# Optimization experiments

Measured on AMD Instinct MI355X. Metric: run time of the kernel, lower is better.

## Reference

```python
import jax, jax.numpy as jnp
import numpy as np

B, T, E, H = 16, 2048, 1024, 128


def setup_inputs() -> dict:
    key = jax.random.key(0)
    kx, kk, kq, kv = jax.random.split(key, 4)
    x = jax.random.normal(kx, (B, T, E), dtype=jnp.float32)
    Wk = jax.random.normal(kk, (E, H), dtype=jnp.float32) / np.sqrt(E)
    Wq = jax.random.normal(kq, (E, H), dtype=jnp.float32) / np.sqrt(E)
    Wv = jax.random.normal(kv, (E, H), dtype=jnp.float32) / np.sqrt(E)
    mask = jnp.tril(jnp.ones((T, T), dtype=jnp.int32))  # causal mask; 0 => blocked
    return {"x": x, "mask": mask, "Wk": Wk, "Wq": Wq, "Wv": Wv}


def reference(x, mask, Wk, Wq, Wv):
    # k, q, v projections (Linear without bias)
    k = x @ Wk  # [B, T, H]
    q = x @ Wq
    v = x @ Wv
    scale = 1.0 / jnp.sqrt(jnp.asarray(H, dtype=x.dtype))
    wei = jnp.einsum("bth,bsh->bts", q, k) * scale  # [B, T, T]
    neg_inf = jnp.asarray(-jnp.inf, dtype=wei.dtype)
    wei = jnp.where(mask == 0, neg_inf, wei)
    wei = jax.nn.softmax(wei, axis=-1)
    out = jnp.einsum("bts,bsh->bth", wei, v)  # [B, T, H]
    return out
```

## Files before the change

kernel.cpp:

```cpp
#include <hip/hip_runtime.h>
#include <hip/hip_bf16.h>
#include <stdint.h>

typedef __attribute__((ext_vector_type(8))) short bf16x8;
typedef __attribute__((ext_vector_type(16))) float f32x16;
typedef __attribute__((ext_vector_type(4))) float f32x4;

__device__ __forceinline__ uint32_t cvt_pk_bf16(float a, float b){
  uint32_t r;
  asm volatile("v_cvt_pk_bf16_f32 %0, %1, %2" : "=v"(r) : "v"(a), "v"(b));
  return r;
}
__device__ __forceinline__ void permswap32(uint32_t &a, uint32_t &b){
  asm volatile("v_permlane32_swap_b32 %0, %1" : "+v"(a), "+v"(b));
}
__device__ __forceinline__ unsigned short f2bf(float f){
  uint32_t u = __float_as_uint(f);
  u += 0x7fff + ((u >> 16) & 1);
  return (unsigned short)(u >> 16);
}


__global__ void prep_w(const float* __restrict__ Wk, const float* __restrict__ Wq,
                       const float* __restrict__ Wv, unsigned short* __restrict__ Wt){
  int idx = blockIdx.x * 256 + threadIdx.x;
  int mat = idx >> 17;
  int r = idx & 131071;
  int h = r & 127;
  int e = r >> 7;
  const float* src = (mat == 0) ? Wq : (mat == 1) ? Wk : Wv;
  float v = src[r];
  if (mat == 0) v *= (1.4426950408889634f * 0.08838834764831845f);
  Wt[(mat * 128 + h) * 1024 + e] = f2bf(v);
}

#define LS 40
__global__ __launch_bounds__(256, 2) void proj_gemm(
    const float* __restrict__ x, const unsigned short* __restrict__ Wt,
    unsigned short* __restrict__ Qb, unsigned short* __restrict__ Kb,
    unsigned short* __restrict__ Vt){
  __shared__ __align__(16) unsigned short As[64 * LS];
  __shared__ __align__(16) unsigned short Bs[384 * LS];
  const int tid  = threadIdx.x;
  const int lane = tid & 63;
  const int w    = tid >> 6;
  const int lr   = lane & 15;
  const int lk   = lane >> 4;
  const int m0   = blockIdx.x * 64;

  f32x4 acc[4][6];
  #pragma unroll
  for (int i = 0; i < 4; ++i)
    #pragma unroll
    for (int jj = 0; jj < 6; ++jj) acc[i][jj] = (f32x4){0.f, 0.f, 0.f, 0.f};

  float4 areg[2];
  bf16x8 breg[6];
  #pragma unroll
  for (int i = 0; i < 2; ++i){
    int idx = i * 256 + tid; int row = idx >> 3, kp = idx & 7;
    areg[i] = *(const float4*)(x + (size_t)(m0 + row) * 1024 + kp * 4);
  }
  #pragma unroll
  for (int i = 0; i < 6; ++i){
    int idx = i * 256 + tid; int row = idx >> 2, pp = idx & 3;
    breg[i] = *(const bf16x8*)(Wt + (size_t)row * 1024 + pp * 8);
  }

  for (int ks = 0; ks < 32; ++ks){
    __syncthreads();
    #pragma unroll
    for (int i = 0; i < 2; ++i){
      int idx = i * 256 + tid; int row = idx >> 3, kp = idx & 7;
      uint32_t lo = cvt_pk_bf16(areg[i].x, areg[i].y);
      uint32_t hi = cvt_pk_bf16(areg[i].z, areg[i].w);
      *(uint2*)((char*)As + row * (LS * 2) + kp * 8) = make_uint2(lo, hi);
    }
    #pragma unroll
    for (int i = 0; i < 6; ++i){
      int idx = i * 256 + tid; int row = idx >> 2, pp = idx & 3;
      *(bf16x8*)((char*)Bs + row * (LS * 2) + pp * 16) = breg[i];
    }
    __syncthreads();
    if (ks + 1 < 32){
      int ko = (ks + 1) * 32;
      #pragma unroll
      for (int i = 0; i < 2; ++i){
        int idx = i * 256 + tid; int row = idx >> 3, kp = idx & 7;
        areg[i] = *(const float4*)(x + (size_t)(m0 + row) * 1024 + ko + kp * 4);
      }
      #pragma unroll
      for (int i = 0; i < 6; ++i){
        int idx = i * 256 + tid; int row = idx >> 2, pp = idx & 3;
        breg[i] = *(const bf16x8*)(Wt + (size_t)row * 1024 + ko + pp * 8);
      }
    }
    bf16x8 af[4], bfr[6];
    #pragma unroll
    for (int am = 0; am < 4; ++am)
      af[am] = *(const bf16x8*)((char*)As + (am * 16 + lr) * (LS * 2) + lk * 16);
    #pragma unroll
    for (int bn = 0; bn < 6; ++bn)
      bfr[bn] = *(const bf16x8*)((char*)Bs + (w * 96 + bn * 16 + lr) * (LS * 2) + lk * 16);
    #pragma unroll
    for (int am = 0; am < 4; ++am)
      #pragma unroll
      for (int bn = 0; bn < 6; ++bn)
        acc[am][bn] = __builtin_amdgcn_mfma_f32_16x16x32_bf16(af[am], bfr[bn], acc[am][bn], 0, 0, 0);
  }

  const int b  = m0 >> 11;
  const int t0 = m0 & 2047;
  #pragma unroll
  for (int am = 0; am < 4; ++am){
    #pragma unroll
    for (int bn = 0; bn < 6; ++bn){
      int c0   = w * 96 + bn * 16;
      int mat  = c0 >> 7;
      int hcol = (c0 & 127) + lr;
      int tr   = t0 + am * 16 + lk * 4;
      f32x4 v = acc[am][bn];
      if (mat <= 1){
        unsigned short* dst = (mat == 0) ? Qb : Kb;
        size_t base = (size_t)(b * 64 + (tr >> 5)) * 4096 + (size_t)(hcol >> 4) * 512 + (hcol & 15);
        #pragma unroll
        for (int jj = 0; jj < 4; ++jj)
          dst[base + (size_t)((tr + jj) & 31) * 16] = f2bf(v[jj]);
      } else {
        ushort4 pk;
        pk.x = f2bf(v[0]); pk.y = f2bf(v[1]); pk.z = f2bf(v[2]); pk.w = f2bf(v[3]);
        size_t addr = (size_t)((b * 64 + (tr >> 5)) * 4 + (hcol >> 5)) * 1024
                    + (size_t)((tr >> 4) & 1) * 512 + (size_t)(hcol & 31) * 16 + (tr & 15);
        *(ushort4*)(Vt + addr) = pk;
      }
    }
  }
}

__global__ __launch_bounds__(256, 2) void attn(
    const unsigned short* __restrict__ Qf, const unsigned short* __restrict__ Kf,
    const unsigned short* __restrict__ Vf, float* __restrict__ out){
  __shared__ float comb[32][132];
  __shared__ float msh[4][32];
  __shared__ float lsh[4][32];

  const int tid  = threadIdx.x;
  const int lane = tid & 63;
  const int w    = tid >> 6;
  const int bid  = blockIdx.x;
  const int xcd  = bid & 7;
  const int k    = bid >> 3;
  const int a    = k & 31;
  const int mdx  = k >> 5;
  const int b    = xcd * 2 + (mdx >> 1);
  const int c    = (mdx & 1) ? a : 63 - a;
  const int r0   = c * 32;
  const int q5   = lane & 31;
  const int hi   = lane >> 5;

  bf16x8 qf[8];
  const unsigned short* qp = Qf + (size_t)(b * 64 + c) * 4096 + q5 * 16 + hi * 8;
  #pragma unroll
  for (int f = 0; f < 8; ++f) qf[f] = *(const bf16x8*)(qp + f * 512);

  f32x16 oacc[4];
  #pragma unroll
  for (int i = 0; i < 4; ++i) oacc[i] = (f32x16)(0.f);
  float m = -1e30f, l = 0.f;

  const unsigned short* kb = Kf + (size_t)b * 64 * 4096;
  const unsigned short* vb = Vf + (size_t)b * 64 * 4096;

  bf16x8 kf[8];
  if (w <= c){
    const unsigned short* kp = kb + (size_t)w * 4096 + q5 * 16 + hi * 8;
    #pragma unroll
    for (int f = 0; f < 8; ++f) kf[f] = *(const bf16x8*)(kp + f * 512);
  }

  for (int t = w; t <= c; t += 4){
    f32x16 sacc = (f32x16)(0.f);
    #pragma unroll
    for (int f = 0; f < 8; ++f)
      sacc = __builtin_amdgcn_mfma_f32_32x32x16_bf16(kf[f], qf[f], sacc, 0, 0, 0);
    if (t + 4 <= c){
      const unsigned short* kp = kb + (size_t)(t + 4) * 4096 + q5 * 16 + hi * 8;
      #pragma unroll
      for (int f = 0; f < 8; ++f) kf[f] = *(const bf16x8*)(kp + f * 512);
    }
    bf16x8 vf[8];
    const unsigned short* vp = vb + (size_t)t * 4096 + q5 * 16 + hi * 8;
    #pragma unroll
    for (int ht = 0; ht < 4; ++ht)
      #pragma unroll
      for (int sf = 0; sf < 2; ++sf)
        vf[ht * 2 + sf] = *(const bf16x8*)(vp + ht * 1024 + sf * 512);

    float sv[16];
    #pragma unroll
    for (int r = 0; r < 16; ++r) sv[r] = sacc[r];
    if (t == c){
      #pragma unroll
      for (int r = 0; r < 16; ++r){
        int srow = (r & 3) + 8 * (r >> 2) + 4 * hi;
        if (srow > q5) sv[r] = -1e30f;
      }
    }
    float pm = sv[0];
    #pragma unroll
    for (int r = 1; r < 16; ++r) pm = fmaxf(pm, sv[r]);
    pm = fmaxf(pm, __shfl_xor(pm, 32));
    if (!__all(pm - m <= 8.0f)){
      float mn = fmaxf(m, pm);
      float al = exp2f(m - mn);
      #pragma unroll
      for (int i = 0; i < 4; ++i) oacc[i] *= al;
      l *= al;
      m = mn;
    }
    float pv[16]; float ts = 0.f;
    #pragma unroll
    for (int r = 0; r < 16; ++r){ pv[r] = exp2f(sv[r] - m); ts += pv[r]; }
    ts += __shfl_xor(ts, 32);
    l += ts;
    uint32_t w0 = cvt_pk_bf16(pv[0],  pv[1]);
    uint32_t w2 = cvt_pk_bf16(pv[4],  pv[5]);  permswap32(w0, w2);
    uint32_t w1 = cvt_pk_bf16(pv[2],  pv[3]);
    uint32_t w3 = cvt_pk_bf16(pv[6],  pv[7]);  permswap32(w1, w3);
    uint32_t w4 = cvt_pk_bf16(pv[8],  pv[9]);
    uint32_t w6 = cvt_pk_bf16(pv[12], pv[13]); permswap32(w4, w6);
    uint32_t w5 = cvt_pk_bf16(pv[10], pv[11]);
    uint32_t w7 = cvt_pk_bf16(pv[14], pv[15]); permswap32(w5, w7);
    union { uint32_t u[4]; bf16x8 v; } pf0u, pf1u;
    pf0u.u[0] = w0; pf0u.u[1] = w1; pf0u.u[2] = w2; pf0u.u[3] = w3;
    pf1u.u[0] = w4; pf1u.u[1] = w5; pf1u.u[2] = w6; pf1u.u[3] = w7;
    #pragma unroll
    for (int ht = 0; ht < 4; ++ht){
      oacc[ht] = __builtin_amdgcn_mfma_f32_32x32x16_bf16(vf[ht * 2 + 0], pf0u.v, oacc[ht], 0, 0, 0);
      oacc[ht] = __builtin_amdgcn_mfma_f32_32x32x16_bf16(vf[ht * 2 + 1], pf1u.v, oacc[ht], 0, 0, 0);
    }
  }

  if (hi == 0){ msh[w][q5] = m; lsh[w][q5] = l; }
  __syncthreads();
  {
    float mv0 = msh[0][q5], mv1 = msh[1][q5], mv2 = msh[2][q5], mv3 = msh[3][q5];
    float lv0 = lsh[0][q5], lv1 = lsh[1][q5], lv2 = lsh[2][q5], lv3 = lsh[3][q5];
    float mfm = fmaxf(fmaxf(mv0, mv1), fmaxf(mv2, mv3));
    float lf  = lv0 * exp2f(mv0 - mfm) + lv1 * exp2f(mv1 - mfm)
              + lv2 * exp2f(mv2 - mfm) + lv3 * exp2f(mv3 - mfm);
    float s = exp2f(m - mfm) / lf;
    #pragma unroll
    for (int ht = 0; ht < 4; ++ht) oacc[ht] *= s;
  }
  #pragma unroll 1
  for (int rr = 0; rr < 4; ++rr){
    if (w == rr){
      #pragma unroll
      for (int ht = 0; ht < 4; ++ht)
        #pragma unroll
        for (int r4 = 0; r4 < 4; ++r4){
          int hh = ht * 32 + 8 * r4 + 4 * hi;
          float4 add;
          add.x = oacc[ht][r4 * 4 + 0]; add.y = oacc[ht][r4 * 4 + 1];
          add.z = oacc[ht][r4 * 4 + 2]; add.w = oacc[ht][r4 * 4 + 3];
          float* p = &comb[q5][hh];
          if (rr == 0) *(float4*)p = add;
          else { float4 cur = *(const float4*)p;
                 cur.x += add.x; cur.y += add.y; cur.z += add.z; cur.w += add.w;
                 *(float4*)p = cur; }
        }
    }
    __syncthreads();
  }
  float* obase = out + ((size_t)b * 2048 + r0) * 128;
  #pragma unroll
  for (int it = 0; it < 4; ++it){
    int row = it * 8 + (tid >> 5);
    int col = (tid & 31) * 4;
    *(float4*)(obase + row * 128 + col) = *(const float4*)&comb[row][col];
  }
}

extern "C" void kernel_launch(void* const* d_in, const int* in_sizes, int n_in,
                              void* d_out, int out_size, void* d_ws, size_t ws_size,
                              hipStream_t stream){
  const float* x  = (const float*)d_in[0];
  const float* Wk = (const float*)d_in[2];
  const float* Wq = (const float*)d_in[3];
  const float* Wv = (const float*)d_in[4];
  char* ws = (char*)d_ws;
  unsigned short* Wt = (unsigned short*)(ws);
  unsigned short* Qb = (unsigned short*)(ws + (1ull  << 20));
  unsigned short* Kb = (unsigned short*)(ws + (9ull  << 20));
  unsigned short* Vt = (unsigned short*)(ws + (17ull << 20));
  float* out = (float*)d_out;

  hipLaunchKernelGGL(prep_w,    dim3(1536), dim3(256), 0, stream, Wk, Wq, Wv, Wt);
  hipLaunchKernelGGL(proj_gemm, dim3(512),  dim3(256), 0, stream, x, Wt, Qb, Kb, Vt);
  hipLaunchKernelGGL(attn,      dim3(1024), dim3(256), 0, stream, Qb, Kb, Vt, out);
}
```

Baseline: 89.07 us.

## Pre-swizzle weights into MFMA fragment layout and drop LDS staging in projection GEMM

The weight prep kernel now writes W in a fragment-tiled order, so each lane can load its bf16x8 MFMA operand straight from global memory. The projection GEMM drops shared memory and both barriers per k-step. Each wave loads its own x rows and weight fragments directly into registers, double-buffered in registers. The M tile is halved to 32 rows, the grid doubles to 1024 blocks, and launch bounds rise to 3 blocks per CU. This removes LDS traffic and synchronisation, at the cost of x being reloaded redundantly by all four waves and more global and L2 traffic for the weights.

```diff
diff --git a/kernel.cpp b/kernel.cpp
--- a/kernel.cpp
+++ b/kernel.cpp
@@ -24,95 +24,110 @@
 __global__ void prep_w(const float* __restrict__ Wk, const float* __restrict__ Wq,
                        const float* __restrict__ Wv, unsigned short* __restrict__ Wt){
   int idx = blockIdx.x * 256 + threadIdx.x;
-  int mat = idx >> 17;
-  int r = idx & 131071;
-  int h = r & 127;
-  int e = r >> 7;
+  int fid = idx >> 9;
+  int within = idx & 511;
+  int nlo = within >> 5;
+  int elo = within & 31;
+  int kq = fid / 24;
+  int nq = fid - kq * 24;
+  int n  = nq * 16 + nlo;
+  int e  = kq * 32 + elo;
+  int mat = n >> 7;
+  int h   = n & 127;
   const float* src = (mat == 0) ? Wq : (mat == 1) ? Wk : Wv;
-  float v = src[r];
+  float v = src[e * 128 + h];
   if (mat == 0) v *= (1.4426950408889634f * 0.08838834764831845f);
-  Wt[(mat * 128 + h) * 1024 + e] = f2bf(v);
-}
-
-#define LS 40
-__global__ __launch_bounds__(256, 2) void proj_gemm(
+  Wt[idx] = f2bf(v);
+}
+
+__global__ __launch_bounds__(256, 3) void proj_gemm(
     const float* __restrict__ x, const unsigned short* __restrict__ Wt,
     unsigned short* __restrict__ Qb, unsigned short* __restrict__ Kb,
     unsigned short* __restrict__ Vt){
-  __shared__ __align__(16) unsigned short As[64 * LS];
-  __shared__ __align__(16) unsigned short Bs[384 * LS];
   const int tid  = threadIdx.x;
   const int lane = tid & 63;
   const int w    = tid >> 6;
   const int lr   = lane & 15;
   const int lk   = lane >> 4;
-  const int m0   = blockIdx.x * 64;
-
-  f32x4 acc[4][6];
-  #pragma unroll
-  for (int i = 0; i < 4; ++i)
+  const int m0   = blockIdx.x * 32;
+
+  f32x4 acc[2][6];
+  #pragma unroll
+  for (int i = 0; i < 2; ++i)
     #pragma unroll
     for (int jj = 0; jj < 6; ++jj) acc[i][jj] = (f32x4){0.f, 0.f, 0.f, 0.f};
 
-  float4 areg[2];
-  bf16x8 breg[6];
-  #pragma unroll
-  for (int i = 0; i < 2; ++i){
-    int idx = i * 256 + tid; int row = idx >> 3, kp = idx & 7;
-    areg[i] = *(const float4*)(x + (size_t)(m0 + row) * 1024 + kp * 4);
-  }
-  #pragma unroll
-  for (int i = 0; i < 6; ++i){
-    int idx = i * 256 + tid; int row = idx >> 2, pp = idx & 3;
-    breg[i] = *(const bf16x8*)(Wt + (size_t)row * 1024 + pp * 8);
+  const float* xp = x + (size_t)(m0 + lr) * 1024 + lk * 8;
+  const unsigned short* bp = Wt + lr * 32 + lk * 8;
+
+  union BU { uint32_t u[4]; bf16x8 v; };
+
+  bf16x8 af0, af1, bcur0, bcur1, bcur2, bcur3, bcur4, bcur5;
+  {
+    float4 a00 = *(const float4*)(xp);
+    float4 a01 = *(const float4*)(xp + 4);
+    float4 a10 = *(const float4*)(xp + 16 * 1024);
+    float4 a11 = *(const float4*)(xp + 16 * 1024 + 4);
+    const unsigned short* bk = bp + (size_t)(w * 6) * 512;
+    bcur0 = *(const bf16x8*)(bk + 0 * 512);
+    bcur1 = *(const bf16x8*)(bk + 1 * 512);
+    bcur2 = *(const bf16x8*)(bk + 2 * 512);
+    bcur3 = *(const bf16x8*)(bk + 3 * 512);
+    bcur4 = *(const bf16x8*)(bk + 4 * 512);
+    bcur5 = *(const bf16x8*)(bk + 5 * 512);
+    BU u0; u0.u[0] = cvt_pk_bf16(a00.x, a00.y); u0.u[1] = cvt_pk_bf16(a00.z, a00.w);
+           u0.u[2] = cvt_pk_bf16(a01.x, a01.y); u0.u[3] = cvt_pk_bf16(a01.z, a01.w);
+    af0 = u0.v;
+    BU u1; u1.u[0] = cvt_pk_bf16(a10.x, a10.y); u1.u[1] = cvt_pk_bf16(a10.z, a10.w);
+           u1.u[2] = cvt_pk_bf16(a11.x, a11.y); u1.u[3] = cvt_pk_bf16(a11.z, a11.w);
+    af1 = u1.v;
   }
 
   for (int ks = 0; ks < 32; ++ks){
-    __syncthreads();
-    #pragma unroll
-    for (int i = 0; i < 2; ++i){
-      int idx = i * 256 + tid; int row = idx >> 3, kp = idx & 7;
-      uint32_t lo = cvt_pk_bf16(areg[i].x, areg[i].y);
-      uint32_t hi = cvt_pk_bf16(areg[i].z, areg[i].w);
-      *(uint2*)((char*)As + row * (LS * 2) + kp * 8) = make_uint2(lo, hi);
-    }
-    #pragma unroll
-    for (int i = 0; i < 6; ++i){
-      int idx = i * 256 + tid; int row = idx >> 2, pp = idx & 3;
-      *(bf16x8*)((char*)Bs + row * (LS * 2) + pp * 16) = breg[i];
-    }
-    __syncthreads();
-    if (ks + 1 < 32){
-      int ko = (ks + 1) * 32;
-      #pragma unroll
-      for (int i = 0; i < 2; ++i){
-        int idx = i * 256 + tid; int row = idx >> 3, kp = idx & 7;
-        areg[i] = *(const float4*)(x + (size_t)(m0 + row) * 1024 + ko + kp * 4);
-      }
-      #pragma unroll
-      for (int i = 0; i < 6; ++i){
-        int idx = i * 256 + tid; int row = idx >> 2, pp = idx & 3;
-        breg[i] = *(const bf16x8*)(Wt + (size_t)row * 1024 + ko + pp * 8);
-      }
-    }
-    bf16x8 af[4], bfr[6];
-    #pragma unroll
-    for (int am = 0; am < 4; ++am)
-      af[am] = *(const bf16x8*)((char*)As + (am * 16 + lr) * (LS * 2) + lk * 16);
-    #pragma unroll
-    for (int bn = 0; bn < 6; ++bn)
-      bfr[bn] = *(const bf16x8*)((char*)Bs + (w * 96 + bn * 16 + lr) * (LS * 2) + lk * 16);
-    #pragma unroll
-    for (int am = 0; am < 4; ++am)
-      #pragma unroll
-      for (int bn = 0; bn < 6; ++bn)
-        acc[am][bn] = __builtin_amdgcn_mfma_f32_16x16x32_bf16(af[am], bfr[bn], acc[am][bn], 0, 0, 0);
+    float4 a00, a01, a10, a11;
+    bf16x8 bn0, bn1, bn2, bn3, bn4, bn5;
+    const bool more = (ks + 1) < 32;
+    if (more){
+      const float* xk = xp + (ks + 1) * 32;
+      a00 = *(const float4*)(xk);
+      a01 = *(const float4*)(xk + 4);
+      a10 = *(const float4*)(xk + 16 * 1024);
+      a11 = *(const float4*)(xk + 16 * 1024 + 4);
+      const unsigned short* bk = bp + (size_t)((ks + 1) * 24 + w * 6) * 512;
+      bn0 = *(const bf16x8*)(bk + 0 * 512);
+      bn1 = *(const bf16x8*)(bk + 1 * 512);
+      bn2 = *(const bf16x8*)(bk + 2 * 512);
+      bn3 = *(const bf16x8*)(bk + 3 * 512);
+      bn4 = *(const bf16x8*)(bk + 4 * 512);
+      bn5 = *(const bf16x8*)(bk + 5 * 512);
+    }
+    acc[0][0] = __builtin_amdgcn_mfma_f32_16x16x32_bf16(af0, bcur0, acc[0][0], 0, 0, 0);
+    acc[1][0] = __builtin_amdgcn_mfma_f32_16x16x32_bf16(af1, bcur0, acc[1][0], 0, 0, 0);
+    acc[0][1] = __builtin_amdgcn_mfma_f32_16x16x32_bf16(af0, bcur1, acc[0][1], 0, 0, 0);
+    acc[1][1] = __builtin_amdgcn_mfma_f32_16x16x32_bf16(af1, bcur1, acc[1][1], 0, 0, 0);
+    acc[0][2] = __builtin_amdgcn_mfma_f32_16x16x32_bf16(af0, bcur2, acc[0][2], 0, 0, 0);
+    acc[1][2] = __builtin_amdgcn_mfma_f32_16x16x32_bf16(af1, bcur2, acc[1][2], 0, 0, 0);
+    acc[0][3] = __builtin_amdgcn_mfma_f32_16x16x32_bf16(af0, bcur3, acc[0][3], 0, 0, 0);
+    acc[1][3] = __builtin_amdgcn_mfma_f32_16x16x32_bf16(af1, bcur3, acc[1][3], 0, 0, 0);
+    acc[0][4] = __builtin_amdgcn_mfma_f32_16x16x32_bf16(af0, bcur4, acc[0][4], 0, 0, 0);
+    acc[1][4] = __builtin_amdgcn_mfma_f32_16x16x32_bf16(af1, bcur4, acc[1][4], 0, 0, 0);
+    acc[0][5] = __builtin_amdgcn_mfma_f32_16x16x32_bf16(af0, bcur5, acc[0][5], 0, 0, 0);
+    acc[1][5] = __builtin_amdgcn_mfma_f32_16x16x32_bf16(af1, bcur5, acc[1][5], 0, 0, 0);
+    if (more){
+      BU u0; u0.u[0] = cvt_pk_bf16(a00.x, a00.y); u0.u[1] = cvt_pk_bf16(a00.z, a00.w);
+             u0.u[2] = cvt_pk_bf16(a01.x, a01.y); u0.u[3] = cvt_pk_bf16(a01.z, a01.w);
+      af0 = u0.v;
+      BU u1; u1.u[0] = cvt_pk_bf16(a10.x, a10.y); u1.u[1] = cvt_pk_bf16(a10.z, a10.w);
+             u1.u[2] = cvt_pk_bf16(a11.x, a11.y); u1.u[3] = cvt_pk_bf16(a11.z, a11.w);
+      af1 = u1.v;
+      bcur0 = bn0; bcur1 = bn1; bcur2 = bn2; bcur3 = bn3; bcur4 = bn4; bcur5 = bn5;
+    }
   }
 
   const int b  = m0 >> 11;
   const int t0 = m0 & 2047;
   #pragma unroll
-  for (int am = 0; am < 4; ++am){
+  for (int am = 0; am < 2; ++am){
     #pragma unroll
     for (int bn = 0; bn < 6; ++bn){
       int c0   = w * 96 + bn * 16;
@@ -297,6 +312,6 @@
   float* out = (float*)d_out;
 
   hipLaunchKernelGGL(prep_w,    dim3(1536), dim3(256), 0, stream, Wk, Wq, Wv, Wt);
-  hipLaunchKernelGGL(proj_gemm, dim3(512),  dim3(256), 0, stream, x, Wt, Qb, Kb, Vt);
+  hipLaunchKernelGGL(proj_gemm, dim3(1024), dim3(256), 0, stream, x, Wt, Qb, Kb, Vt);
   hipLaunchKernelGGL(attn,      dim3(1024), dim3(256), 0, stream, Qb, Kb, Vt, out);
 }
```

Result: slower. 148.9 us (+67.1%).

## Stream projection GEMM tiles via direct global-to-LDS loads with multi-buffering

Applied to the files above, without the earlier changes.

The projection GEMM now copies x and the weight tiles straight into LDS with global_load_lds, replacing the register-staged loads and LDS stores. x uses a triple buffer and Wt a double buffer, so only one barrier per k-step is needed and loads overlap MFMA work. prep_w now writes the weights pre-swizzled into MFMA fragment order, and the fp32 x is converted to bf16 after the LDS read. The change also raises wave priority around the MFMA block. In exchange LDS use grows, which may limit occupancy, and the hand-written vmcnt waits must exactly match the number of loads in flight.

```diff
diff --git a/kernel.cpp b/kernel.cpp
--- a/kernel.cpp
+++ b/kernel.cpp
@@ -19,33 +19,41 @@
   u += 0x7fff + ((u >> 16) & 1);
   return (unsigned short)(u >> 16);
 }
+__device__ __forceinline__ void gload16(const void* g, void* l){
+  __builtin_amdgcn_global_load_lds((const __attribute__((address_space(1))) void*)g,
+                                   (__attribute__((address_space(3))) void*)l, 16, 0, 0);
+}
 
 
 __global__ void prep_w(const float* __restrict__ Wk, const float* __restrict__ Wq,
                        const float* __restrict__ Wv, unsigned short* __restrict__ Wt){
   int idx = blockIdx.x * 256 + threadIdx.x;
-  int mat = idx >> 17;
-  int r = idx & 131071;
-  int h = r & 127;
-  int e = r >> 7;
+  int frag = idx >> 9;
+  int r    = idx & 511;
+  int ln   = r >> 3;
+  int j    = r & 7;
+  int kq = frag / 24;
+  int nq = frag - kq * 24;
+  int n  = nq * 16 + (ln & 15);
+  int e  = kq * 32 + (ln >> 4) * 8 + j;
+  int mat = n >> 7;
+  int h   = n & 127;
   const float* src = (mat == 0) ? Wq : (mat == 1) ? Wk : Wv;
-  float v = src[r];
+  float v = src[e * 128 + h];
   if (mat == 0) v *= (1.4426950408889634f * 0.08838834764831845f);
-  Wt[(mat * 128 + h) * 1024 + e] = f2bf(v);
-}
-
-#define LS 40
+  Wt[idx] = f2bf(v);
+}
+
 __global__ __launch_bounds__(256, 2) void proj_gemm(
     const float* __restrict__ x, const unsigned short* __restrict__ Wt,
     unsigned short* __restrict__ Qb, unsigned short* __restrict__ Kb,
     unsigned short* __restrict__ Vt){
-  __shared__ __align__(16) unsigned short As[64 * LS];
-  __shared__ __align__(16) unsigned short Bs[384 * LS];
+  __shared__ __align__(16) float          As[3][2048];
+  __shared__ __align__(16) unsigned short Bs[2][12288];
+
   const int tid  = threadIdx.x;
   const int lane = tid & 63;
   const int w    = tid >> 6;
-  const int lr   = lane & 15;
-  const int lk   = lane >> 4;
   const int m0   = blockIdx.x * 64;
 
   f32x4 acc[4][6];
@@ -54,63 +62,70 @@
     #pragma unroll
     for (int jj = 0; jj < 6; ++jj) acc[i][jj] = (f32x4){0.f, 0.f, 0.f, 0.f};
 
-  float4 areg[2];
-  bf16x8 breg[6];
-  #pragma unroll
-  for (int i = 0; i < 2; ++i){
-    int idx = i * 256 + tid; int row = idx >> 3, kp = idx & 7;
-    areg[i] = *(const float4*)(x + (size_t)(m0 + row) * 1024 + kp * 4);
-  }
-  #pragma unroll
-  for (int i = 0; i < 6; ++i){
-    int idx = i * 256 + tid; int row = idx >> 2, pp = idx & 3;
-    breg[i] = *(const bf16x8*)(Wt + (size_t)row * 1024 + pp * 8);
-  }
+  const int lt0 = (lane >> 1), lt1 = 32 + (lane >> 1);
+  const int arow0 = w * 16 + (lt0 & 15), akk0 = (lt0 >> 4) * 8 + (lane & 1) * 4;
+  const int arow1 = w * 16 + (lt1 & 15), akk1 = (lt1 >> 4) * 8 + (lane & 1) * 4;
+  const float* asrc0 = x + (size_t)(m0 + arow0) * 1024 + akk0;
+  const float* asrc1 = x + (size_t)(m0 + arow1) * 1024 + akk1;
+  const unsigned short* bsrc = Wt + (size_t)lane * 8;
+
+  #define STAGE_A(kt, buf) {                                              \
+    gload16(asrc0 + (kt) * 32, &As[buf][(2 * w + 0) * 256]);              \
+    gload16(asrc1 + (kt) * 32, &As[buf][(2 * w + 1) * 256]);              \
+  }
+  #define STAGE_B(kt, buf) {                                              \
+    _Pragma("unroll")                                                     \
+    for (int jf = 0; jf < 6; ++jf){                                       \
+      int f = w * 6 + jf;                                                 \
+      gload16(bsrc + ((size_t)(kt) * 24 + f) * 512, &Bs[buf][f * 512]);   \
+    }                                                                     \
+  }
+
+  union BU { uint32_t u[4]; bf16x8 v; };
+
+  STAGE_B(0, 0);
+  STAGE_A(0, 0);
+  STAGE_A(1, 1);
+  asm volatile("s_waitcnt vmcnt(2)" ::: "memory");
+  __builtin_amdgcn_s_barrier();
+  __builtin_amdgcn_sched_barrier(0);
 
   for (int ks = 0; ks < 32; ++ks){
-    __syncthreads();
-    #pragma unroll
-    for (int i = 0; i < 2; ++i){
-      int idx = i * 256 + tid; int row = idx >> 3, kp = idx & 7;
-      uint32_t lo = cvt_pk_bf16(areg[i].x, areg[i].y);
-      uint32_t hi = cvt_pk_bf16(areg[i].z, areg[i].w);
-      *(uint2*)((char*)As + row * (LS * 2) + kp * 8) = make_uint2(lo, hi);
-    }
-    #pragma unroll
-    for (int i = 0; i < 6; ++i){
-      int idx = i * 256 + tid; int row = idx >> 2, pp = idx & 3;
-      *(bf16x8*)((char*)Bs + row * (LS * 2) + pp * 16) = breg[i];
-    }
-    __syncthreads();
-    if (ks + 1 < 32){
-      int ko = (ks + 1) * 32;
-      #pragma unroll
-      for (int i = 0; i < 2; ++i){
-        int idx = i * 256 + tid; int row = idx >> 3, kp = idx & 7;
-        areg[i] = *(const float4*)(x + (size_t)(m0 + row) * 1024 + ko + kp * 4);
-      }
-      #pragma unroll
-      for (int i = 0; i < 6; ++i){
-        int idx = i * 256 + tid; int row = idx >> 2, pp = idx & 3;
-        breg[i] = *(const bf16x8*)(Wt + (size_t)row * 1024 + ko + pp * 8);
-      }
-    }
-    bf16x8 af[4], bfr[6];
+    const int bcur = ks & 1, bnxt = bcur ^ 1;
+    const int acur = ks % 3, anxt2 = (ks + 2) % 3;
+    const int kb = (ks + 1 < 32) ? ks + 1 : 31;
+    const int ka = (ks + 2 < 32) ? ks + 2 : 31;
+    STAGE_B(kb, bnxt);
+    STAGE_A(ka, anxt2);
+    bf16x8 af[4];
+    #pragma unroll
+    for (int am = 0; am < 4; ++am){
+      float4 lo = *(const float4*)&As[acur][am * 512 + lane * 8];
+      float4 hi = *(const float4*)&As[acur][am * 512 + lane * 8 + 4];
+      BU u; u.u[0] = cvt_pk_bf16(lo.x, lo.y); u.u[1] = cvt_pk_bf16(lo.z, lo.w);
+            u.u[2] = cvt_pk_bf16(hi.x, hi.y); u.u[3] = cvt_pk_bf16(hi.z, hi.w);
+      af[am] = u.v;
+    }
+    bf16x8 bf[6];
+    #pragma unroll
+    for (int bn = 0; bn < 6; ++bn)
+      bf[bn] = *(const bf16x8*)&Bs[bcur][(w * 6 + bn) * 512 + lane * 8];
+    __builtin_amdgcn_s_setprio(1);
     #pragma unroll
     for (int am = 0; am < 4; ++am)
-      af[am] = *(const bf16x8*)((char*)As + (am * 16 + lr) * (LS * 2) + lk * 16);
-    #pragma unroll
-    for (int bn = 0; bn < 6; ++bn)
-      bfr[bn] = *(const bf16x8*)((char*)Bs + (w * 96 + bn * 16 + lr) * (LS * 2) + lk * 16);
-    #pragma unroll
-    for (int am = 0; am < 4; ++am)
       #pragma unroll
       for (int bn = 0; bn < 6; ++bn)
-        acc[am][bn] = __builtin_amdgcn_mfma_f32_16x16x32_bf16(af[am], bfr[bn], acc[am][bn], 0, 0, 0);
+        acc[am][bn] = __builtin_amdgcn_mfma_f32_16x16x32_bf16(af[am], bf[bn], acc[am][bn], 0, 0, 0);
+    __builtin_amdgcn_s_setprio(0);
+    asm volatile("s_waitcnt vmcnt(2)" ::: "memory");
+    __builtin_amdgcn_s_barrier();
+    __builtin_amdgcn_sched_barrier(0);
   }
 
   const int b  = m0 >> 11;
   const int t0 = m0 & 2047;
+  const int lr = lane & 15;
+  const int lk = lane >> 4;
   #pragma unroll
   for (int am = 0; am < 4; ++am){
     #pragma unroll
@@ -135,6 +150,8 @@
       }
     }
   }
+  #undef STAGE_A
+  #undef STAGE_B
 }
 
 __global__ __launch_bounds__(256, 2) void attn(
```

Result: no change. 89.43 us (+0.4%).
